# Optimization experiments

Measured on AMD Instinct MI355X. Metric: run time of the kernel, lower is better.

Reference implementation:

```python
import jax, jax.numpy as jnp
import numpy as np

B, S, D_MODEL, H = 2, 2048, 1024, 16
DH = D_MODEL // H  # 64


def setup_inputs() -> dict:
    key = jax.random.key(0)
    ks = jax.random.split(key, 12)
    sc = 1.0 / np.sqrt(D_MODEL)
    inp = {
        "q": jax.random.normal(ks[0], (B, S, D_MODEL), jnp.float32),
        "k": jax.random.normal(ks[1], (B, S, D_MODEL), jnp.float32),
        "v": jax.random.normal(ks[2], (B, S, D_MODEL), jnp.float32),
        # causal mask, broadcast over batch and heads; 0 entries get -inf
        "mask": jnp.tril(jnp.ones((S, S), jnp.int32))[None, None],
        "wq": jax.random.normal(ks[3], (D_MODEL, D_MODEL), jnp.float32) * sc,
        "bq": jax.random.normal(ks[4], (D_MODEL,), jnp.float32) * sc,
        "wk": jax.random.normal(ks[5], (D_MODEL, D_MODEL), jnp.float32) * sc,
        "bk": jax.random.normal(ks[6], (D_MODEL,), jnp.float32) * sc,
        "wv": jax.random.normal(ks[7], (D_MODEL, D_MODEL), jnp.float32) * sc,
        "bv": jax.random.normal(ks[8], (D_MODEL,), jnp.float32) * sc,
        "wo": jax.random.normal(ks[9], (D_MODEL, D_MODEL), jnp.float32) * sc,
        "bo": jax.random.normal(ks[10], (D_MODEL,), jnp.float32) * sc,
    }
    return inp


def reference(q, k, v, mask, wq, bq, wk, bk, wv, bv, wo, bo):
    # nn.Linear: y = x @ W.T + b
    def proj(x, w, b):
        y = jnp.einsum('bsd,ed->bse', x, w) + b
        return y.reshape(B, -1, H, DH).transpose(0, 2, 1, 3)  # [B,H,S,DH]

    qh = proj(q, wq, bq)
    kh = proj(k, wk, bk)
    vh = proj(v, wv, bv)

    scores = jnp.einsum('bhqd,bhkd->bhqk', qh, kh) / jnp.sqrt(jnp.float32(DH))
    scores = jnp.where(mask == 0, jnp.float32(-jnp.inf), scores)
    attn = jax.nn.softmax(scores, axis=-1)  # dropout_rate=0.0 -> identity

    ctx = jnp.einsum('bhqk,bhkd->bhqd', attn, vh)
    ctx = ctx.transpose(0, 2, 1, 3).reshape(B, -1, D_MODEL)
    out = jnp.einsum('bsd,ed->bse', ctx, wo) + bo
    return out, attn
```

## Files before the change

kernel.cpp:

```cpp
#include <hip/hip_runtime.h>
#include <hip/hip_bf16.h>
#include <cstdint>

#define S_LEN  2048
#define DMODEL 1024
#define NHEAD  16
#define NBATCH 2
#define OUT_ELEMS (NBATCH * S_LEN * DMODEL)

#define WS_XQ   0
#define WS_XK   8388608
#define WS_XV   16777216
#define WS_WQ   25165824
#define WS_WK   27262976
#define WS_WV   29360128
#define WS_WO   31457280
#define WS_QH   33554432
#define WS_KH   41943040
#define WS_VH   50331648
#define WS_CTX  58720256

typedef __attribute__((ext_vector_type(8))) short short8;
typedef __attribute__((ext_vector_type(4))) short short4v;
typedef __attribute__((ext_vector_type(4))) float f32x4;

typedef __attribute__((address_space(1))) const void gvoid_t;
typedef __attribute__((address_space(3))) void lvoid_t;

__device__ __forceinline__ short f2bf(float f) {
  __hip_bfloat16 h = __float2bfloat16(f);
  return __builtin_bit_cast(short, h);
}

__device__ __forceinline__ void gload_lds16(const void* g, void* l) {
  __builtin_amdgcn_global_load_lds((gvoid_t*)g, (lvoid_t*)l, 16, 0, 0);
}

__global__ void conv_x(const float* __restrict__ q, const float* __restrict__ k,
                       const float* __restrict__ v, short* __restrict__ xq,
                       short* __restrict__ xk, short* __restrict__ xv) {
  int i = blockIdx.x * 256 + threadIdx.x;
  const float* in = blockIdx.y == 0 ? q : blockIdx.y == 1 ? k : v;
  short* out = blockIdx.y == 0 ? xq : blockIdx.y == 1 ? xk : xv;
  float4 val = ((const float4*)in)[i];
  short4v o;
  o[0] = f2bf(val.x); o[1] = f2bf(val.y); o[2] = f2bf(val.z); o[3] = f2bf(val.w);
  ((short4v*)out)[i] = o;
}

__global__ void conv_w(const float* __restrict__ a, const float* __restrict__ b,
                       const float* __restrict__ c, const float* __restrict__ d,
                       short* __restrict__ oa, short* __restrict__ ob,
                       short* __restrict__ oc, short* __restrict__ od) {
  int i = blockIdx.x * 256 + threadIdx.x;
  const float* in = blockIdx.y == 0 ? a : blockIdx.y == 1 ? b : blockIdx.y == 2 ? c : d;
  short* out = blockIdx.y == 0 ? oa : blockIdx.y == 1 ? ob : blockIdx.y == 2 ? oc : od;
  float4 val = ((const float4*)in)[i];
  short4v o;
  o[0] = f2bf(val.x); o[1] = f2bf(val.y); o[2] = f2bf(val.z); o[3] = f2bf(val.w);
  ((short4v*)out)[i] = o;
}

__device__ __forceinline__ void gemm_core(const short* __restrict__ A, const short* __restrict__ Wt,
                                          short* Als, short* Wls, f32x4 (&acc)[4][4]) {
  const int tid = threadIdx.x, lane = tid & 63, wid = tid >> 6;
  const int wr = wid >> 1, wc = wid & 1;
  const int l15 = lane & 15, l4 = lane >> 4;
  const int r_in = lane >> 2, c8 = (lane & 3) * 8;

  for (int k0 = 0; k0 < DMODEL; k0 += 32) {
#pragma unroll
    for (int i = 0; i < 2; ++i) {
      int ch = wid * 2 + i;
      gload_lds16(A + (size_t)(ch * 16 + r_in) * DMODEL + k0 + c8, &Als[ch * 512]);
      gload_lds16(Wt + (size_t)(ch * 16 + r_in) * DMODEL + k0 + c8, &Wls[ch * 512]);
    }
    __syncthreads();
    short8 af[4], bf[4];
    const int ko = l4 * 8;
#pragma unroll
    for (int mt = 0; mt < 4; ++mt)
      af[mt] = *(const short8*)&Als[(wr * 64 + mt * 16 + l15) * 32 + ko];
#pragma unroll
    for (int nt = 0; nt < 4; ++nt)
      bf[nt] = *(const short8*)&Wls[(wc * 64 + nt * 16 + l15) * 32 + ko];
#pragma unroll
    for (int mt = 0; mt < 4; ++mt)
#pragma unroll
      for (int nt = 0; nt < 4; ++nt)
        acc[mt][nt] = __builtin_amdgcn_mfma_f32_16x16x32_bf16(af[mt], bf[nt], acc[mt][nt], 0, 0, 0);
    __syncthreads();
  }
}

__global__ __launch_bounds__(256, 2)
void gemm_proj(char* __restrict__ ws, const float* __restrict__ bq,
               const float* __restrict__ bk, const float* __restrict__ bv) {
  __shared__ short Als[128 * 32];
  __shared__ short Wls[128 * 32];
  const int sel = blockIdx.y;
  const short* A  = (const short*)(ws + (sel == 0 ? WS_XQ : sel == 1 ? WS_XK : WS_XV));
  const short* Wt = (const short*)(ws + (sel == 0 ? WS_WQ : sel == 1 ? WS_WK : WS_WV));
  const float* bias = sel == 0 ? bq : sel == 1 ? bk : bv;
  short* Cb = (short*)(ws + (sel == 0 ? WS_QH : sel == 1 ? WS_KH : WS_VH));

  const int bm = blockIdx.x / 8, bn = blockIdx.x % 8;
  const int tid = threadIdx.x, lane = tid & 63, wid = tid >> 6;
  const int wr = wid >> 1, wc = wid & 1;
  const int l15 = lane & 15, l4 = lane >> 4;

  f32x4 zero4 = {0.f, 0.f, 0.f, 0.f};
  f32x4 acc[4][4];
#pragma unroll
  for (int mt = 0; mt < 4; ++mt)
#pragma unroll
    for (int nt = 0; nt < 4; ++nt) acc[mt][nt] = zero4;

  gemm_core(A + (size_t)(bm * 128) * DMODEL, Wt + (size_t)(bn * 128) * DMODEL, Als, Wls, acc);

#pragma unroll
  for (int nt = 0; nt < 4; ++nt) {
    int n = bn * 128 + wc * 64 + nt * 16 + l15;
    float bvl = bias[n];
    int h = n >> 6, dh = n & 63;
#pragma unroll
    for (int mt = 0; mt < 4; ++mt) {
#pragma unroll
      for (int r = 0; r < 4; ++r) {
        int m = bm * 128 + wr * 64 + mt * 16 + l4 * 4 + r;
        int b = m >> 11, s = m & (S_LEN - 1);
        Cb[(((size_t)b * NHEAD + h) * S_LEN + s) * 64 + dh] = f2bf(acc[mt][nt][r] + bvl);
      }
    }
  }
}

__global__ __launch_bounds__(256, 2)
void gemm_out(const short* __restrict__ A, const short* __restrict__ Wt,
              const float* __restrict__ bias, float* __restrict__ Cf) {
  __shared__ short Als[128 * 32];
  __shared__ short Wls[128 * 32];
  const int bm = blockIdx.x / 8, bn = blockIdx.x % 8;
  const int tid = threadIdx.x, lane = tid & 63, wid = tid >> 6;
  const int wr = wid >> 1, wc = wid & 1;
  const int l15 = lane & 15, l4 = lane >> 4;

  f32x4 zero4 = {0.f, 0.f, 0.f, 0.f};
  f32x4 acc[4][4];
#pragma unroll
  for (int mt = 0; mt < 4; ++mt)
#pragma unroll
    for (int nt = 0; nt < 4; ++nt) acc[mt][nt] = zero4;

  gemm_core(A + (size_t)(bm * 128) * DMODEL, Wt + (size_t)(bn * 128) * DMODEL, Als, Wls, acc);

#pragma unroll
  for (int nt = 0; nt < 4; ++nt) {
    int n = bn * 128 + wc * 64 + nt * 16 + l15;
    float bvl = bias[n];
#pragma unroll
    for (int mt = 0; mt < 4; ++mt) {
#pragma unroll
      for (int r = 0; r < 4; ++r) {
        int m = bm * 128 + wr * 64 + mt * 16 + l4 * 4 + r;
        Cf[(size_t)m * DMODEL + n] = acc[mt][nt][r] + bvl;
      }
    }
  }
}

__global__ __launch_bounds__(256, 2)
void attn_fused(const short* __restrict__ Qh, const short* __restrict__ Kh,
                const short* __restrict__ Vh, float* __restrict__ attn,
                short* __restrict__ ctx) {
  __shared__ short Vt[64 * 64];
  __shared__ short Pls[64 * 64];

  const int bid = blockIdx.x;
  const int xcd = bid & 7, slot = bid >> 3;
  const int bh = xcd * 4 + (slot >> 4);
  const int p = slot & 15;

  const int tid = threadIdx.x, lane = tid & 63, wid = tid >> 6;
  const int l15 = lane & 15, l4 = lane >> 4;
  const size_t hoff = (size_t)bh * S_LEN * 64;
  const short* Kb = Kh + hoff;
  const short* Vb = Vh + hoff;
  const int b = bh >> 4, h = bh & 15;

  f32x4 zero4 = {0.f, 0.f, 0.f, 0.f};

#pragma unroll 1
  for (int half = 0; half < 2; ++half) {
    const int bx = half ? 31 - p : p;
    const int q0 = bx * 64;
    const short* Qb = Qh + hoff + (size_t)q0 * 64;
    float* arow = attn + ((size_t)bh * S_LEN + q0) * S_LEN;

    short8 qf[2];
#pragma unroll
    for (int kh = 0; kh < 2; ++kh)
      qf[kh] = *(const short8*)&Qb[(wid * 16 + l15) * 64 + kh * 32 + l4 * 8];

    float l[4] = {0.f, 0.f, 0.f, 0.f};
#pragma unroll 1
    for (int kt = 0; kt <= bx; ++kt) {
      f32x4 acc[4];
#pragma unroll
      for (int nt = 0; nt < 4; ++nt) acc[nt] = zero4;
#pragma unroll
      for (int kh = 0; kh < 2; ++kh) {
#pragma unroll
        for (int nt = 0; nt < 4; ++nt) {
          short8 bf = *(const short8*)&Kb[(size_t)(kt * 64 + nt * 16 + l15) * 64 + kh * 32 + l4 * 8];
          acc[nt] = __builtin_amdgcn_mfma_f32_16x16x32_bf16(qf[kh], bf, acc[nt], 0, 0, 0);
        }
      }
#pragma unroll
      for (int r = 0; r < 4; ++r) {
#pragma unroll
        for (int nt = 0; nt < 4; ++nt) {
          float s = acc[nt][r] * 0.125f;
          if (kt == bx) {
            int keyl = nt * 16 + l15, ql = wid * 16 + l4 * 4 + r;
            if (keyl > ql) s = -INFINITY;
          }
          l[r] += __expf(s);
        }
      }
    }
    float rinv[4];
#pragma unroll
    for (int r = 0; r < 4; ++r) {
      float t = l[r];
#pragma unroll
      for (int msk = 1; msk < 16; msk <<= 1) t += __shfl_xor(t, msk, 64);
      rinv[r] = 1.f / t;
    }

#pragma unroll 1
    for (int kt = bx + 1; kt < S_LEN / 64; ++kt) {
      float4 z = {0.f, 0.f, 0.f, 0.f};
#pragma unroll
      for (int i = 0; i < 4; ++i) {
        int c = tid * 4 + i;
        int row = c >> 4, c4 = (c & 15) * 4;
        *(float4*)&arow[(size_t)row * S_LEN + kt * 64 + c4] = z;
      }
    }

    f32x4 cacc[4];
#pragma unroll
    for (int nt = 0; nt < 4; ++nt) cacc[nt] = zero4;

#pragma unroll 1
    for (int kt = 0; kt <= bx; ++kt) {
      f32x4 acc[4];
#pragma unroll
      for (int nt = 0; nt < 4; ++nt) acc[nt] = zero4;
#pragma unroll
      for (int kh = 0; kh < 2; ++kh) {
#pragma unroll
        for (int nt = 0; nt < 4; ++nt) {
          short8 bf = *(const short8*)&Kb[(size_t)(kt * 64 + nt * 16 + l15) * 64 + kh * 32 + l4 * 8];
          acc[nt] = __builtin_amdgcn_mfma_f32_16x16x32_bf16(qf[kh], bf, acc[nt], 0, 0, 0);
        }
      }
      float pv[4][4];
#pragma unroll
      for (int nt = 0; nt < 4; ++nt) {
#pragma unroll
        for (int r = 0; r < 4; ++r) {
          float s = acc[nt][r] * 0.125f;
          if (kt == bx) {
            int keyl = nt * 16 + l15, ql = wid * 16 + l4 * 4 + r;
            if (keyl > ql) s = -INFINITY;
          }
          float pp = __expf(s) * rinv[r];
          pv[nt][r] = pp;
          arow[(size_t)(wid * 16 + l4 * 4 + r) * S_LEN + kt * 64 + nt * 16 + l15] = pp;
        }
      }
      __syncthreads();
#pragma unroll
      for (int nt = 0; nt < 4; ++nt)
#pragma unroll
        for (int r = 0; r < 4; ++r)
          Pls[(wid * 16 + l4 * 4 + r) * 64 + nt * 16 + l15] = f2bf(pv[nt][r]);
#pragma unroll
      for (int i = 0; i < 2; ++i) {
        int c = tid * 2 + i;
        int kk = c >> 3, d0 = (c & 7) * 8;
        short8 v8 = *(const short8*)&Vb[(size_t)(kt * 64 + kk) * 64 + d0];
#pragma unroll
        for (int j = 0; j < 8; ++j) Vt[(d0 + j) * 64 + kk] = v8[j];
      }
      __syncthreads();
#pragma unroll
      for (int kh = 0; kh < 2; ++kh) {
        short8 pa = *(const short8*)&Pls[(wid * 16 + l15) * 64 + kh * 32 + l4 * 8];
#pragma unroll
        for (int nt = 0; nt < 4; ++nt) {
          short8 vf = *(const short8*)&Vt[(nt * 16 + l15) * 64 + kh * 32 + l4 * 8];
          cacc[nt] = __builtin_amdgcn_mfma_f32_16x16x32_bf16(pa, vf, cacc[nt], 0, 0, 0);
        }
      }
    }

#pragma unroll
    for (int nt = 0; nt < 4; ++nt) {
#pragma unroll
      for (int r = 0; r < 4; ++r) {
        int q = q0 + wid * 16 + l4 * 4 + r;
        int d = nt * 16 + l15;
        ctx[((size_t)b * S_LEN + q) * DMODEL + h * 64 + d] = f2bf(cacc[nt][r]);
      }
    }
  }
}

extern "C" void kernel_launch(void* const* d_in, const int* in_sizes, int n_in,
                              void* d_out, int out_size, void* d_ws, size_t ws_size,
                              hipStream_t stream) {
  const float* q  = (const float*)d_in[0];
  const float* k  = (const float*)d_in[1];
  const float* v  = (const float*)d_in[2];
  const float* wq = (const float*)d_in[4];
  const float* bq = (const float*)d_in[5];
  const float* wk = (const float*)d_in[6];
  const float* bk = (const float*)d_in[7];
  const float* wv = (const float*)d_in[8];
  const float* bv = (const float*)d_in[9];
  const float* wo = (const float*)d_in[10];
  const float* bo = (const float*)d_in[11];

  char* ws = (char*)d_ws;
  short* Xq  = (short*)(ws + WS_XQ);
  short* Xk  = (short*)(ws + WS_XK);
  short* Xv  = (short*)(ws + WS_XV);
  short* Wqb = (short*)(ws + WS_WQ);
  short* Wkb = (short*)(ws + WS_WK);
  short* Wvb = (short*)(ws + WS_WV);
  short* Wob = (short*)(ws + WS_WO);
  short* Qhp = (short*)(ws + WS_QH);
  short* Khp = (short*)(ws + WS_KH);
  short* Vhp = (short*)(ws + WS_VH);
  short* Ctx = (short*)(ws + WS_CTX);

  float* out_f  = (float*)d_out;
  float* attn_f = out_f + OUT_ELEMS;

  conv_x<<<dim3(OUT_ELEMS / 4 / 256, 3), 256, 0, stream>>>(q, k, v, Xq, Xk, Xv);
  conv_w<<<dim3(DMODEL * DMODEL / 4 / 256, 4), 256, 0, stream>>>(wq, wk, wv, wo, Wqb, Wkb, Wvb, Wob);

  gemm_proj<<<dim3(256, 3), 256, 0, stream>>>(ws, bq, bk, bv);

  attn_fused<<<512, 256, 0, stream>>>(Qhp, Khp, Vhp, attn_f, Ctx);

  gemm_out<<<256, 256, 0, stream>>>(Ctx, Wob, bo, out_f);
}
```

Before: 835.9 us.

## Write V head-transposed from projection and drop block barriers in attention

The V projection now swaps the MFMA operands so each lane holds a column, and stores V as [b,h,dh,s]. This lets attention read V fragments straight from global memory instead of transposing them through shared memory. Attention now keeps P in a per-wave swizzled LDS region, with only an lgkmcnt wait instead of two block-wide barriers per key tile. The kernel also launches one block per query tile (1024 blocks, 4 per CU) instead of pairing tiles inside a block, which removes the load balancing that pairing gave a causal workload.

```diff
diff --git a/kernel.cpp b/kernel.cpp
--- a/kernel.cpp
+++ b/kernel.cpp
@@ -61,6 +61,7 @@
   ((short4v*)out)[i] = o;
 }
 
+template <bool SWAP>
 __device__ __forceinline__ void gemm_core(const short* __restrict__ A, const short* __restrict__ Wt,
                                           short* Als, short* Wls, f32x4 (&acc)[4][4]) {
   const int tid = threadIdx.x, lane = tid & 63, wid = tid >> 6;
@@ -87,8 +88,12 @@
 #pragma unroll
     for (int mt = 0; mt < 4; ++mt)
 #pragma unroll
-      for (int nt = 0; nt < 4; ++nt)
-        acc[mt][nt] = __builtin_amdgcn_mfma_f32_16x16x32_bf16(af[mt], bf[nt], acc[mt][nt], 0, 0, 0);
+      for (int nt = 0; nt < 4; ++nt) {
+        if (SWAP)
+          acc[mt][nt] = __builtin_amdgcn_mfma_f32_16x16x32_bf16(bf[nt], af[mt], acc[mt][nt], 0, 0, 0);
+        else
+          acc[mt][nt] = __builtin_amdgcn_mfma_f32_16x16x32_bf16(af[mt], bf[nt], acc[mt][nt], 0, 0, 0);
+      }
     __syncthreads();
   }
 }
@@ -116,20 +121,41 @@
 #pragma unroll
     for (int nt = 0; nt < 4; ++nt) acc[mt][nt] = zero4;
 
-  gemm_core(A + (size_t)(bm * 128) * DMODEL, Wt + (size_t)(bn * 128) * DMODEL, Als, Wls, acc);
-
-#pragma unroll
-  for (int nt = 0; nt < 4; ++nt) {
-    int n = bn * 128 + wc * 64 + nt * 16 + l15;
-    float bvl = bias[n];
-    int h = n >> 6, dh = n & 63;
-#pragma unroll
-    for (int mt = 0; mt < 4; ++mt) {
+  const short* Ab = A + (size_t)(bm * 128) * DMODEL;
+  const short* Wb = Wt + (size_t)(bn * 128) * DMODEL;
+
+  if (sel < 2) {
+    gemm_core<false>(Ab, Wb, Als, Wls, acc);
+#pragma unroll
+    for (int nt = 0; nt < 4; ++nt) {
+      int n = bn * 128 + wc * 64 + nt * 16 + l15;
+      float bvl = bias[n];
+      int h = n >> 6, dh = n & 63;
+#pragma unroll
+      for (int mt = 0; mt < 4; ++mt) {
+#pragma unroll
+        for (int r = 0; r < 4; ++r) {
+          int m = bm * 128 + wr * 64 + mt * 16 + l4 * 4 + r;
+          int b = m >> 11, s = m & (S_LEN - 1);
+          Cb[(((size_t)b * NHEAD + h) * S_LEN + s) * 64 + dh] = f2bf(acc[mt][nt][r] + bvl);
+        }
+      }
+    }
+  } else {
+    gemm_core<true>(Ab, Wb, Als, Wls, acc);
+#pragma unroll
+    for (int nt = 0; nt < 4; ++nt) {
 #pragma unroll
       for (int r = 0; r < 4; ++r) {
-        int m = bm * 128 + wr * 64 + mt * 16 + l4 * 4 + r;
-        int b = m >> 11, s = m & (S_LEN - 1);
-        Cb[(((size_t)b * NHEAD + h) * S_LEN + s) * 64 + dh] = f2bf(acc[mt][nt][r] + bvl);
+        int n = bn * 128 + wc * 64 + nt * 16 + l4 * 4 + r;
+        float bvl = bias[n];
+        int h = n >> 6, dh = n & 63;
+#pragma unroll
+        for (int mt = 0; mt < 4; ++mt) {
+          int m = bm * 128 + wr * 64 + mt * 16 + l15;
+          int b = m >> 11, s = m & (S_LEN - 1);
+          Cb[((size_t)(b * NHEAD + h) * 64 + dh) * S_LEN + s] = f2bf(acc[mt][nt][r] + bvl);
+        }
       }
     }
   }
@@ -152,7 +178,7 @@
 #pragma unroll
     for (int nt = 0; nt < 4; ++nt) acc[mt][nt] = zero4;
 
-  gemm_core(A + (size_t)(bm * 128) * DMODEL, Wt + (size_t)(bn * 128) * DMODEL, Als, Wls, acc);
+  gemm_core<false>(A + (size_t)(bm * 128) * DMODEL, Wt + (size_t)(bn * 128) * DMODEL, Als, Wls, acc);
 
 #pragma unroll
   for (int nt = 0; nt < 4; ++nt) {
@@ -169,152 +195,135 @@
   }
 }
 
-__global__ __launch_bounds__(256, 2)
+__global__ __launch_bounds__(256, 4)
 void attn_fused(const short* __restrict__ Qh, const short* __restrict__ Kh,
-                const short* __restrict__ Vh, float* __restrict__ attn,
+                const short* __restrict__ Vth, float* __restrict__ attn,
                 short* __restrict__ ctx) {
-  __shared__ short Vt[64 * 64];
-  __shared__ short Pls[64 * 64];
+  __shared__ short Pls[4 * 1024];
 
   const int bid = blockIdx.x;
   const int xcd = bid & 7, slot = bid >> 3;
-  const int bh = xcd * 4 + (slot >> 4);
-  const int p = slot & 15;
+  const int bh = xcd * 4 + (slot >> 5);
+  const int bx = slot & 31;
+  const int q0 = bx * 64;
 
   const int tid = threadIdx.x, lane = tid & 63, wid = tid >> 6;
   const int l15 = lane & 15, l4 = lane >> 4;
   const size_t hoff = (size_t)bh * S_LEN * 64;
   const short* Kb = Kh + hoff;
-  const short* Vb = Vh + hoff;
+  const short* Vb = Vth + hoff;
+  const short* Qb = Qh + hoff + (size_t)q0 * 64;
+  float* arow = attn + ((size_t)bh * S_LEN + q0) * S_LEN;
+  char* Pwb = (char*)&Pls[wid * 1024];
+
+  f32x4 zero4 = {0.f, 0.f, 0.f, 0.f};
+
+  short8 qf[2];
+#pragma unroll
+  for (int kh = 0; kh < 2; ++kh)
+    qf[kh] = *(const short8*)&Qb[(wid * 16 + l15) * 64 + kh * 32 + l4 * 8];
+
+  float l[4] = {0.f, 0.f, 0.f, 0.f};
+#pragma unroll 1
+  for (int kt = 0; kt <= bx; ++kt) {
+    f32x4 acc[4];
+#pragma unroll
+    for (int nt = 0; nt < 4; ++nt) acc[nt] = zero4;
+#pragma unroll
+    for (int kh = 0; kh < 2; ++kh) {
+#pragma unroll
+      for (int nt = 0; nt < 4; ++nt) {
+        short8 bf = *(const short8*)&Kb[(size_t)(kt * 64 + nt * 16 + l15) * 64 + kh * 32 + l4 * 8];
+        acc[nt] = __builtin_amdgcn_mfma_f32_16x16x32_bf16(qf[kh], bf, acc[nt], 0, 0, 0);
+      }
+    }
+#pragma unroll
+    for (int r = 0; r < 4; ++r) {
+#pragma unroll
+      for (int nt = 0; nt < 4; ++nt) {
+        float s = acc[nt][r] * 0.125f;
+        if (kt == bx) {
+          int keyl = nt * 16 + l15, ql = wid * 16 + l4 * 4 + r;
+          if (keyl > ql) s = -INFINITY;
+        }
+        l[r] += __expf(s);
+      }
+    }
+  }
+  float rinv[4];
+#pragma unroll
+  for (int r = 0; r < 4; ++r) {
+    float t = l[r];
+#pragma unroll
+    for (int msk = 1; msk < 16; msk <<= 1) t += __shfl_xor(t, msk, 64);
+    rinv[r] = 1.f / t;
+  }
+
+#pragma unroll 1
+  for (int kt = bx + 1; kt < S_LEN / 64; ++kt) {
+    float4 z = {0.f, 0.f, 0.f, 0.f};
+#pragma unroll
+    for (int i = 0; i < 4; ++i) {
+      int c = tid * 4 + i;
+      int row = c >> 4, c4 = (c & 15) * 4;
+      *(float4*)&arow[(size_t)row * S_LEN + kt * 64 + c4] = z;
+    }
+  }
+
+  f32x4 cacc[4];
+#pragma unroll
+  for (int nt = 0; nt < 4; ++nt) cacc[nt] = zero4;
+
+#pragma unroll 1
+  for (int kt = 0; kt <= bx; ++kt) {
+    f32x4 acc[4];
+#pragma unroll
+    for (int nt = 0; nt < 4; ++nt) acc[nt] = zero4;
+#pragma unroll
+    for (int kh = 0; kh < 2; ++kh) {
+#pragma unroll
+      for (int nt = 0; nt < 4; ++nt) {
+        short8 bf = *(const short8*)&Kb[(size_t)(kt * 64 + nt * 16 + l15) * 64 + kh * 32 + l4 * 8];
+        acc[nt] = __builtin_amdgcn_mfma_f32_16x16x32_bf16(qf[kh], bf, acc[nt], 0, 0, 0);
+      }
+    }
+#pragma unroll
+    for (int nt = 0; nt < 4; ++nt) {
+#pragma unroll
+      for (int r = 0; r < 4; ++r) {
+        float s = acc[nt][r] * 0.125f;
+        if (kt == bx) {
+          int keyl = nt * 16 + l15, ql = wid * 16 + l4 * 4 + r;
+          if (keyl > ql) s = -INFINITY;
+        }
+        float pp = __expf(s) * rinv[r];
+        arow[(size_t)(wid * 16 + l4 * 4 + r) * S_LEN + kt * 64 + nt * 16 + l15] = pp;
+        int row = l4 * 4 + r;
+        int wb = (row * 128 + (nt * 16 + l15) * 2) ^ ((row & 7) << 4);
+        *(short*)(Pwb + wb) = f2bf(pp);
+      }
+    }
+    asm volatile("s_waitcnt lgkmcnt(0)" ::: "memory");
+#pragma unroll
+    for (int kh = 0; kh < 2; ++kh) {
+      int rb = (l15 * 128 + kh * 64 + l4 * 16) ^ ((l15 & 7) << 4);
+      short8 pa = *(const short8*)(Pwb + rb);
+#pragma unroll
+      for (int nt = 0; nt < 4; ++nt) {
+        short8 vf = *(const short8*)&Vb[(size_t)(nt * 16 + l15) * S_LEN + kt * 64 + kh * 32 + l4 * 8];
+        cacc[nt] = __builtin_amdgcn_mfma_f32_16x16x32_bf16(pa, vf, cacc[nt], 0, 0, 0);
+      }
+    }
+  }
+
   const int b = bh >> 4, h = bh & 15;
-
-  f32x4 zero4 = {0.f, 0.f, 0.f, 0.f};
-
-#pragma unroll 1
-  for (int half = 0; half < 2; ++half) {
-    const int bx = half ? 31 - p : p;
-    const int q0 = bx * 64;
-    const short* Qb = Qh + hoff + (size_t)q0 * 64;
-    float* arow = attn + ((size_t)bh * S_LEN + q0) * S_LEN;
-
-    short8 qf[2];
-#pragma unroll
-    for (int kh = 0; kh < 2; ++kh)
-      qf[kh] = *(const short8*)&Qb[(wid * 16 + l15) * 64 + kh * 32 + l4 * 8];
-
-    float l[4] = {0.f, 0.f, 0.f, 0.f};
-#pragma unroll 1
-    for (int kt = 0; kt <= bx; ++kt) {
-      f32x4 acc[4];
-#pragma unroll
-      for (int nt = 0; nt < 4; ++nt) acc[nt] = zero4;
-#pragma unroll
-      for (int kh = 0; kh < 2; ++kh) {
-#pragma unroll
-        for (int nt = 0; nt < 4; ++nt) {
-          short8 bf = *(const short8*)&Kb[(size_t)(kt * 64 + nt * 16 + l15) * 64 + kh * 32 + l4 * 8];
-          acc[nt] = __builtin_amdgcn_mfma_f32_16x16x32_bf16(qf[kh], bf, acc[nt], 0, 0, 0);
-        }
-      }
-#pragma unroll
-      for (int r = 0; r < 4; ++r) {
-#pragma unroll
-        for (int nt = 0; nt < 4; ++nt) {
-          float s = acc[nt][r] * 0.125f;
-          if (kt == bx) {
-            int keyl = nt * 16 + l15, ql = wid * 16 + l4 * 4 + r;
-            if (keyl > ql) s = -INFINITY;
-          }
-          l[r] += __expf(s);
-        }
-      }
-    }
-    float rinv[4];
+#pragma unroll
+  for (int nt = 0; nt < 4; ++nt) {
 #pragma unroll
     for (int r = 0; r < 4; ++r) {
-      float t = l[r];
-#pragma unroll
-      for (int msk = 1; msk < 16; msk <<= 1) t += __shfl_xor(t, msk, 64);
-      rinv[r] = 1.f / t;
-    }
-
-#pragma unroll 1
-    for (int kt = bx + 1; kt < S_LEN / 64; ++kt) {
-      float4 z = {0.f, 0.f, 0.f, 0.f};
-#pragma unroll
-      for (int i = 0; i < 4; ++i) {
-        int c = tid * 4 + i;
-        int row = c >> 4, c4 = (c & 15) * 4;
-        *(float4*)&arow[(size_t)row * S_LEN + kt * 64 + c4] = z;
-      }
-    }
-
-    f32x4 cacc[4];
-#pragma unroll
-    for (int nt = 0; nt < 4; ++nt) cacc[nt] = zero4;
-
-#pragma unroll 1
-    for (int kt = 0; kt <= bx; ++kt) {
-      f32x4 acc[4];
-#pragma unroll
-      for (int nt = 0; nt < 4; ++nt) acc[nt] = zero4;
-#pragma unroll
-      for (int kh = 0; kh < 2; ++kh) {
-#pragma unroll
-        for (int nt = 0; nt < 4; ++nt) {
-          short8 bf = *(const short8*)&Kb[(size_t)(kt * 64 + nt * 16 + l15) * 64 + kh * 32 + l4 * 8];
-          acc[nt] = __builtin_amdgcn_mfma_f32_16x16x32_bf16(qf[kh], bf, acc[nt], 0, 0, 0);
-        }
-      }
-      float pv[4][4];
-#pragma unroll
-      for (int nt = 0; nt < 4; ++nt) {
-#pragma unroll
-        for (int r = 0; r < 4; ++r) {
-          float s = acc[nt][r] * 0.125f;
-          if (kt == bx) {
-            int keyl = nt * 16 + l15, ql = wid * 16 + l4 * 4 + r;
-            if (keyl > ql) s = -INFINITY;
-          }
-          float pp = __expf(s) * rinv[r];
-          pv[nt][r] = pp;
-          arow[(size_t)(wid * 16 + l4 * 4 + r) * S_LEN + kt * 64 + nt * 16 + l15] = pp;
-        }
-      }
-      __syncthreads();
-#pragma unroll
-      for (int nt = 0; nt < 4; ++nt)
-#pragma unroll
-        for (int r = 0; r < 4; ++r)
-          Pls[(wid * 16 + l4 * 4 + r) * 64 + nt * 16 + l15] = f2bf(pv[nt][r]);
-#pragma unroll
-      for (int i = 0; i < 2; ++i) {
-        int c = tid * 2 + i;
-        int kk = c >> 3, d0 = (c & 7) * 8;
-        short8 v8 = *(const short8*)&Vb[(size_t)(kt * 64 + kk) * 64 + d0];
-#pragma unroll
-        for (int j = 0; j < 8; ++j) Vt[(d0 + j) * 64 + kk] = v8[j];
-      }
-      __syncthreads();
-#pragma unroll
-      for (int kh = 0; kh < 2; ++kh) {
-        short8 pa = *(const short8*)&Pls[(wid * 16 + l15) * 64 + kh * 32 + l4 * 8];
-#pragma unroll
-        for (int nt = 0; nt < 4; ++nt) {
-          short8 vf = *(const short8*)&Vt[(nt * 16 + l15) * 64 + kh * 32 + l4 * 8];
-          cacc[nt] = __builtin_amdgcn_mfma_f32_16x16x32_bf16(pa, vf, cacc[nt], 0, 0, 0);
-        }
-      }
-    }
-
-#pragma unroll
-    for (int nt = 0; nt < 4; ++nt) {
-#pragma unroll
-      for (int r = 0; r < 4; ++r) {
-        int q = q0 + wid * 16 + l4 * 4 + r;
-        int d = nt * 16 + l15;
-        ctx[((size_t)b * S_LEN + q) * DMODEL + h * 64 + d] = f2bf(cacc[nt][r]);
-      }
+      int q = q0 + wid * 16 + l4 * 4 + r;
+      int d = nt * 16 + l15;
+      ctx[((size_t)b * S_LEN + q) * DMODEL + h * 64 + d] = f2bf(cacc[nt][r]);
     }
   }
 }
@@ -344,7 +353,7 @@
   short* Wob = (short*)(ws + WS_WO);
   short* Qhp = (short*)(ws + WS_QH);
   short* Khp = (short*)(ws + WS_KH);
-  short* Vhp = (short*)(ws + WS_VH);
+  short* Vtp = (short*)(ws + WS_VH);
   short* Ctx = (short*)(ws + WS_CTX);
 
   float* out_f  = (float*)d_out;
@@ -355,7 +364,7 @@
 
   gemm_proj<<<dim3(256, 3), 256, 0, stream>>>(ws, bq, bk, bv);
 
-  attn_fused<<<512, 256, 0, stream>>>(Qhp, Khp, Vhp, attn_f, Ctx);
+  attn_fused<<<1024, 256, 0, stream>>>(Qhp, Khp, Vtp, attn_f, Ctx);
 
   gemm_out<<<256, 256, 0, stream>>>(Ctx, Wob, bo, out_f);
 }
```

Measured after the change: 954.2 us. 1.14x slower.
